# Optimization experiments

Measured on AMD Instinct MI355X. Metric: run time of the kernel, lower is better.

Reference implementation:

```python
import jax, jax.numpy as jnp
import numpy as np


def setup_inputs() -> dict:
    key = jax.random.key(0)
    ks = jax.random.split(key, 10)
    B, S, D = 16, 2048, 256
    return {
        "x": jax.random.normal(ks[0], (B, S, D), dtype=jnp.float32),
        "noise": jax.random.normal(ks[1], (B, S, D), dtype=jnp.float32),
        "alpha1": jax.random.normal(ks[2], (D,), dtype=jnp.float32),
        "alpha2": jax.random.normal(ks[3], (D,), dtype=jnp.float32),
        "W_ttt": jax.random.normal(ks[4], (D, D), dtype=jnp.float32),
        "W_proj": jax.random.normal(ks[5], (D, D), dtype=jnp.float32),
        "ff_alpha": jax.random.normal(ks[6], (D,), dtype=jnp.float32),
        "ff_beta": jax.random.normal(ks[7], (D,), dtype=jnp.float32),
        "ff_gamma": jax.random.normal(ks[8], (1,), dtype=jnp.float32),
        "ff_eta": jax.random.normal(ks[9], (1,), dtype=jnp.float32),
    }


def _ttt(W, m, noise):
    # m, noise: [B, S, D]; sequential SGD on W over the sequence axis.
    B, S, D = m.shape
    scale = 2.0 / (B * D)  # d(mse)/d(pred) factor

    def step(W, inp):
        state, eps = inp                      # [B, D] each
        train = state + eps
        diff = train @ W.T - state            # pred - label, [B, D]
        grad = scale * (diff.T @ train)       # dL/dW, [D, D]
        Wn = W - 0.01 * grad
        return Wn, state @ Wn.T               # readout with updated W

    _, outs = jax.lax.scan(step, W, (jnp.swapaxes(m, 0, 1), jnp.swapaxes(noise, 0, 1)))
    return jnp.swapaxes(outs, 0, 1)           # [B, S, D]


def reference(x, noise, alpha1, alpha2, W_ttt, W_proj, ff_alpha, ff_beta, ff_gamma, ff_eta):
    # memory path: VecDyT norm then TTT (readouts are detached in torch)
    m = jnp.tanh(alpha1 * x)
    mem = jax.lax.stop_gradient(_ttt(W_ttt, m, noise))

    # feedforward path: VecDyT norm then FFUnit
    v = jnp.tanh(alpha2 * x)
    u = ff_gamma * jax.nn.gelu(ff_alpha * v, approximate=False) + ff_eta * jnp.sin(ff_beta * v)
    g = u * (v @ W_proj.T)

    return mem + g
```

## Files before the change

kernel.cpp:

```cpp
#include <hip/hip_runtime.h>

typedef unsigned short u16;
typedef unsigned int u32;
typedef __attribute__((ext_vector_type(8))) short bf16x8;
typedef __attribute__((ext_vector_type(4))) float f32x4;

#define SB 16
#define SS 2048
#define SD 256
#define CC 16
#define NCH (SS / CC)
#define KAPPA 4.8828125e-6f
#define RP 24
#define SLOT 65536

__device__ __forceinline__ u16 f2bf(float f) {
  u32 u = __float_as_uint(f);
  u = (u + 0x7FFFu + ((u >> 16) & 1u)) >> 16;
  return (u16)u;
}
__device__ __forceinline__ float bf2f(u16 u) { return __uint_as_float((u32)u << 16); }

__device__ __forceinline__ bf16x8 ldfrag(const u16* p) {
  union { uint4 u; bf16x8 f; } cv;
  cv.u = *(const uint4*)p;
  return cv.f;
}
__device__ __forceinline__ bf16x8 asfrag(uint4 q) {
  union { uint4 u; bf16x8 f; } cv;
  cv.u = q;
  return cv.f;
}
__device__ __forceinline__ f32x4 mfma16(bf16x8 a, bf16x8 b, f32x4 c) {
  return __builtin_amdgcn_mfma_f32_16x16x32_bf16(a, b, c, 0, 0, 0);
}

__global__ __launch_bounds__(256) void prep_kernel(
    const float* __restrict__ x, const float* __restrict__ noise,
    const float* __restrict__ a1,
    u16* __restrict__ train, u16* __restrict__ state, u16* __restrict__ trainT) {
  size_t i4 = (size_t)blockIdx.x * 256 + threadIdx.x;
  size_t base = i4 * 4;
  int d = (int)(base & 255);
  int t = (int)((base >> 8) & 2047);
  int b = (int)(base >> 19);
  float4 xv = *(const float4*)(x + base);
  float4 nv = *(const float4*)(noise + base);
  float4 av = *(const float4*)(a1 + d);
  float m0 = tanhf(av.x * xv.x);
  float m1 = tanhf(av.y * xv.y);
  float m2 = tanhf(av.z * xv.z);
  float m3 = tanhf(av.w * xv.w);
  size_t dst = ((size_t)t * SB + b) * SD + d;
  ushort4 tr, st;
  tr.x = f2bf(m0 + nv.x); tr.y = f2bf(m1 + nv.y);
  tr.z = f2bf(m2 + nv.z); tr.w = f2bf(m3 + nv.w);
  st.x = f2bf(m0); st.y = f2bf(m1); st.z = f2bf(m2); st.w = f2bf(m3);
  *(ushort4*)(train + dst) = tr;
  *(ushort4*)(state + dst) = st;
  size_t tb = ((size_t)t * SD + d) * SB + b;
  trainT[tb + 0 * SB] = tr.x;
  trainT[tb + 1 * SB] = tr.y;
  trainT[tb + 2 * SB] = tr.z;
  trainT[tb + 3 * SB] = tr.w;
}

__global__ __launch_bounds__(256) void gram2ff_kernel(
    const u16* __restrict__ tr, const u16* __restrict__ st,
    u16* __restrict__ AG, u16* __restrict__ LbG,
    const float* __restrict__ x, const float* __restrict__ a2,
    const float* __restrict__ Wp, const float* __restrict__ ffa,
    const float* __restrict__ ffb, const float* __restrict__ ffg_,
    const float* __restrict__ ffe_, float* __restrict__ out) {
  __shared__ float As[32][68];
  __shared__ float Bs[32][68];
  const int tid = threadIdx.x;

  if (blockIdx.x < 2048) {
    const int cb = blockIdx.x;
    const int c = cb >> 4, t = cb & 15;
    const int lane = tid & 63, wv = tid >> 6;
    const int lr = lane & 15, lq = lane >> 4;
    const size_t Tt = (size_t)cb;
    bf16x8 trF[8], stF[8];
#pragma unroll
    for (int k = 0; k < 8; ++k) {
      trF[k] = ldfrag(tr + (Tt * 16 + lr) * 256 + k * 32 + lq * 8);
      stF[k] = ldfrag(st + (Tt * 16 + lr) * 256 + k * 32 + lq * 8);
    }
    for (int ii = 0; ii < 2; ++ii) {
      const int sp = wv + ii * 4;
      u16* dA = AG + ((size_t)cb * 8 + sp) * 512;
      u16* dL = LbG + ((size_t)cb * 8 + sp) * 512;
#pragma unroll
      for (int h = 0; h < 2; ++h) {
        const int s = 2 * sp + h;
        f32x4 accA = {0.f, 0.f, 0.f, 0.f}, accL = {0.f, 0.f, 0.f, 0.f};
        if (s <= t) {
          const u16* bsrc = tr + ((size_t)(c * 16 + s) * 16 + lr) * 256 + lq * 8;
#pragma unroll
          for (int k = 0; k < 8; ++k) {
            bf16x8 bk = ldfrag(bsrc + k * 32);
            if (s < t) accA = mfma16(trF[k], bk, accA);
            accL = mfma16(stF[k], bk, accL);
          }
        }
#pragma unroll
        for (int r = 0; r < 4; ++r) {
          int idx = (lq * 4 + r) * 32 + h * 16 + lr;
          dA[idx] = (s < t) ? f2bf(accA[r]) : (u16)0;
          dL[idx] = (s <= t) ? f2bf(accL[r]) : (u16)0;
        }
      }
    }
    return;
  }

  const int fb = blockIdx.x - 2048;
  const int gm0 = (fb >> 2) * 64;
  const int gn0 = (fb & 3) * 64;
  const int tm = tid & 15, tn = tid >> 4;
  const int lr = tid & 63;
  const int lq = tid >> 6;
  float acc[4][4];
#pragma unroll
  for (int i = 0; i < 4; i++)
#pragma unroll
    for (int j = 0; j < 4; j++) acc[i][j] = 0.f;

  for (int k0 = 0; k0 < 256; k0 += 32) {
    {
      const float* xp = x + (size_t)(gm0 + lr) * 256 + k0 + lq * 8;
      float4 v0 = *(const float4*)(xp);
      float4 v1 = *(const float4*)(xp + 4);
      const float* ap = a2 + k0 + lq * 8;
      float4 a0 = *(const float4*)(ap);
      float4 a1v = *(const float4*)(ap + 4);
      As[lq * 8 + 0][lr] = tanhf(a0.x * v0.x);
      As[lq * 8 + 1][lr] = tanhf(a0.y * v0.y);
      As[lq * 8 + 2][lr] = tanhf(a0.z * v0.z);
      As[lq * 8 + 3][lr] = tanhf(a0.w * v0.w);
      As[lq * 8 + 4][lr] = tanhf(a1v.x * v1.x);
      As[lq * 8 + 5][lr] = tanhf(a1v.y * v1.y);
      As[lq * 8 + 6][lr] = tanhf(a1v.z * v1.z);
      As[lq * 8 + 7][lr] = tanhf(a1v.w * v1.w);
      const float* wp = Wp + (size_t)(gn0 + lr) * 256 + k0 + lq * 8;
      float4 w0 = *(const float4*)(wp);
      float4 w1 = *(const float4*)(wp + 4);
      Bs[lq * 8 + 0][lr] = w0.x; Bs[lq * 8 + 1][lr] = w0.y;
      Bs[lq * 8 + 2][lr] = w0.z; Bs[lq * 8 + 3][lr] = w0.w;
      Bs[lq * 8 + 4][lr] = w1.x; Bs[lq * 8 + 5][lr] = w1.y;
      Bs[lq * 8 + 6][lr] = w1.z; Bs[lq * 8 + 7][lr] = w1.w;
    }
    __syncthreads();
#pragma unroll
    for (int k = 0; k < 32; ++k) {
      float4 av4 = *(const float4*)&As[k][tm * 4];
      float4 bv4 = *(const float4*)&Bs[k][tn * 4];
      float a[4] = {av4.x, av4.y, av4.z, av4.w};
      float b[4] = {bv4.x, bv4.y, bv4.z, bv4.w};
#pragma unroll
      for (int i = 0; i < 4; i++)
#pragma unroll
        for (int j = 0; j < 4; j++) acc[i][j] += a[i] * b[j];
    }
    __syncthreads();
  }
  const float ga = ffg_[0], et = ffe_[0];
#pragma unroll
  for (int ii = 0; ii < 4; ++ii) {
    int row = gm0 + tm * 4 + ii;
    int col = gn0 + tn * 4;
    float4 xv = *(const float4*)(x + (size_t)row * 256 + col);
    float4 fa = *(const float4*)(ffa + col);
    float4 fb4 = *(const float4*)(ffb + col);
    float4 a2v = *(const float4*)(a2 + col);
    float xs[4] = {xv.x, xv.y, xv.z, xv.w};
    float fas[4] = {fa.x, fa.y, fa.z, fa.w};
    float fbs[4] = {fb4.x, fb4.y, fb4.z, fb4.w};
    float a2s[4] = {a2v.x, a2v.y, a2v.z, a2v.w};
    float res[4];
#pragma unroll
    for (int j = 0; j < 4; ++j) {
      float v = tanhf(a2s[j] * xs[j]);
      float z = fas[j] * v;
      float gelu = 0.5f * z * (1.0f + erff(z * 0.70710678118654752f));
      float u = ga * gelu + et * sinf(fbs[j] * v);
      res[j] = u * acc[ii][j];
    }
    float4 o; o.x = res[0]; o.y = res[1]; o.z = res[2]; o.w = res[3];
    *(float4*)(out + (size_t)row * 256 + col) = o;
  }
}

__global__ __launch_bounds__(512) void phaseA_kernel(
    const u16* __restrict__ tr, const u16* __restrict__ st,
    const u16* __restrict__ trT, const u16* __restrict__ AG,
    u16* __restrict__ Dt, u16* __restrict__ Db, u16* __restrict__ Qb) {
  __shared__ u16 StT[CC][16 * RP];
  __shared__ u16 YtL[CC][16 * RP];
  __shared__ u16 ZtL[CC][16 * RP];
  const int tid = threadIdx.x;
  const int lane = tid & 63;
  const int w = tid >> 6;
  const int d1b = blockIdx.x;
  const int c = blockIdx.y;
  const int lr = lane & 15;
  const int lq = lane >> 4;

  uint4 agR[2][8];
#pragma unroll
  for (int u = 0; u < 2; ++u) {
    const u16* ag = AG + ((size_t)(c * 16 + w + 8 * u) * 8) * 512 + lr * 32 + lq * 8;
#pragma unroll
    for (int sp = 0; sp < 8; ++sp) agR[u][sp] = *(const uint4*)(ag + sp * 512);
  }
  u16 sraw[2][4];
  float xs[2][4];
#pragma unroll
  for (int u = 0; u < 2; ++u) {
    const size_t T = (size_t)c * CC + w + 8 * u;
    ushort4 pk;
#pragma unroll
    for (int r = 0; r < 4; ++r) {
      size_t idx = (T * 16 + lq * 4 + r) * 256 + d1b * 16 + lr;
      sraw[u][r] = st[idx];
      xs[u][r] = bf2f(tr[idx]);
      ((u16*)&pk)[r] = sraw[u][r];
    }
    *(ushort4*)(&StT[w + 8 * u][lr * RP + lq * 4]) = pk;
  }
  __syncthreads();

#pragma unroll
  for (int u = 0; u < 2; ++u) {
    f32x4 a1 = {0.f, 0.f, 0.f, 0.f}, a2 = {0.f, 0.f, 0.f, 0.f};
#pragma unroll
    for (int sp = 0; sp < 8; ++sp) {
      const int s0 = 2 * sp + (lq >> 1);
      bf16x8 xb = ldfrag(trT + ((size_t)(c * CC + s0) * 256 + d1b * 16 + lr) * 16 +
                         (lq & 1) * 8);
      bf16x8 sb = ldfrag(&StT[s0][lr * RP + (lq & 1) * 8]);
      a1 = mfma16(asfrag(agR[u][sp]), xb, a1);
      a2 = mfma16(asfrag(agR[u][sp]), sb, a2);
    }
    ushort4 py, pz;
#pragma unroll
    for (int r = 0; r < 4; ++r) {
      ((u16*)&py)[r] = f2bf(xs[u][r] - KAPPA * a1[r]);
      ((u16*)&pz)[r] = f2bf(bf2f(sraw[u][r]) - KAPPA * a2[r]);
    }
    *(ushort4*)(&YtL[w + 8 * u][lr * RP + lq * 4]) = py;
    *(ushort4*)(&ZtL[w + 8 * u][lr * RP + lq * 4]) = pz;
  }
  __syncthreads();

  bf16x8 yf[8], zf[8];
#pragma unroll
  for (int sp = 0; sp < 8; ++sp) {
    yf[sp] = ldfrag(&YtL[2 * sp + (lq >> 1)][lr * RP + (lq & 1) * 8]);
    zf[sp] = ldfrag(&ZtL[2 * sp + (lq >> 1)][lr * RP + (lq & 1) * 8]);
  }
  const size_t base = (size_t)c * SLOT;
#pragma unroll
  for (int u = 0; u < 2; ++u) {
    const int d2b = w + 8 * u;
    f32x4 da = {0.f, 0.f, 0.f, 0.f}, qa = {0.f, 0.f, 0.f, 0.f};
#pragma unroll
    for (int sp = 0; sp < 8; ++sp) {
      bf16x8 xb = ldfrag(trT + ((size_t)(c * CC + 2 * sp + (lq >> 1)) * 256 +
                                d2b * 16 + lr) * 16 + (lq & 1) * 8);
      da = mfma16(yf[sp], xb, da);
      qa = mfma16(zf[sp], xb, qa);
    }
    ushort4 dpk;
#pragma unroll
    for (int r = 0; r < 4; ++r) {
      const u16 dv = f2bf(-KAPPA * da[r]);
      ((u16*)&dpk)[r] = dv;
      Db[base + (size_t)(d1b * 16 + lq * 4 + r) * 256 + d2b * 16 + lr] = dv;
      Qb[base + (size_t)(d1b * 16 + lq * 4 + r) * 256 + d2b * 16 + lr] =
          f2bf(KAPPA * qa[r]);
    }
    *(ushort4*)(Dt + base + (size_t)(d2b * 16 + lr) * 256 + d1b * 16 + lq * 4) = dpk;
  }
}

__global__ __launch_bounds__(512) void kq_kernel(
    const u16* __restrict__ Dt, u16* __restrict__ Qb, int lev) {
  const int qn = blockIdx.x >> 4, rb = blockIdx.x & 15;
  const int half = 1 << (lev - 1);
  const int blk = qn >> (lev - 1), win = qn & (half - 1);
  const int i = blk * half * 2 + half + win;
  const int j = blk * half * 2 + half - 1;
  u16* Qi = Qb + (size_t)i * SLOT;
  const u16* Qj = Qb + (size_t)j * SLOT;
  const u16* Dti = Dt + (size_t)i * SLOT;
  const int lane = threadIdx.x & 63, w = threadIdx.x >> 6;
  const int lr = lane & 15, lq = lane >> 4;
  bf16x8 aq[8];
#pragma unroll
  for (int kb = 0; kb < 8; ++kb)
    aq[kb] = ldfrag(Qj + (size_t)(rb * 16 + lr) * 256 + kb * 32 + lq * 8);
#pragma unroll
  for (int u = 0; u < 2; ++u) {
    const int cb = w + 8 * u;
    f32x4 acc = {0.f, 0.f, 0.f, 0.f};
#pragma unroll
    for (int kb = 0; kb < 8; ++kb) {
      bf16x8 bf = ldfrag(Dti + (size_t)(cb * 16 + lr) * 256 + kb * 32 + lq * 8);
      acc = mfma16(aq[kb], bf, acc);
    }
#pragma unroll
    for (int r = 0; r < 4; ++r) {
      size_t idx = (size_t)(rb * 16 + lq * 4 + r) * 256 + cb * 16 + lr;
      float v = acc[r] + bf2f(Qj[idx]) + bf2f(Qi[idx]);
      Qi[idx] = f2bf(v);
    }
  }
}

__global__ __launch_bounds__(512) void kdt_kernel(
    u16* __restrict__ Dt, u16* __restrict__ Db, int lev) {
  const int qn = blockIdx.x >> 4, rb = blockIdx.x & 15;
  const int half = 1 << (lev - 1);
  const int blk = qn >> (lev - 1), win = qn & (half - 1);
  const int i = blk * half * 2 + half + win;
  const int j = blk * half * 2 + half - 1;
  u16* Dti = Dt + (size_t)i * SLOT;
  const u16* Dtj = Dt + (size_t)j * SLOT;
  u16* Dbi = Db + (size_t)i * SLOT;
  const u16* Dbj = Db + (size_t)j * SLOT;
  const int lane = threadIdx.x & 63, w = threadIdx.x >> 6;
  const int lr = lane & 15, lq = lane >> 4;
  bf16x8 ad[8];
#pragma unroll
  for (int kb = 0; kb < 8; ++kb)
    ad[kb] = ldfrag(Dti + (size_t)(rb * 16 + lr) * 256 + kb * 32 + lq * 8);
  float oldv[2][4];
#pragma unroll
  for (int u = 0; u < 2; ++u) {
    const int cb = w + 8 * u;
#pragma unroll
    for (int r = 0; r < 4; ++r) {
      size_t idx = (size_t)(rb * 16 + lq * 4 + r) * 256 + cb * 16 + lr;
      oldv[u][r] = bf2f(Dtj[idx]) + bf2f(Dti[idx]);
    }
  }
  __syncthreads();
#pragma unroll
  for (int u = 0; u < 2; ++u) {
    const int cb = w + 8 * u;
    f32x4 acc = {0.f, 0.f, 0.f, 0.f};
#pragma unroll
    for (int kb = 0; kb < 8; ++kb) {
      bf16x8 bf = ldfrag(Dbj + (size_t)(cb * 16 + lr) * 256 + kb * 32 + lq * 8);
      acc = mfma16(ad[kb], bf, acc);
    }
    ushort4 mir;
#pragma unroll
    for (int r = 0; r < 4; ++r) {
      const u16 nv = f2bf(acc[r] + oldv[u][r]);
      ((u16*)&mir)[r] = nv;
      Dti[(size_t)(rb * 16 + lq * 4 + r) * 256 + cb * 16 + lr] = nv;
    }
    *(ushort4*)(Dbi + (size_t)(cb * 16 + lr) * 256 + rb * 16 + lq * 4) = mir;
  }
}

__global__ __launch_bounds__(512) void wstart_kernel(
    const float* __restrict__ Wttt, const u16* __restrict__ Dt,
    const u16* __restrict__ Qb, u16* __restrict__ Wsb) {
  const int c = blockIdx.x;
  const int tid = threadIdx.x;
  const int lane = tid & 63, w = tid >> 6;
  const int lr = lane & 15, lq = lane >> 4;
  if (c == 0) {
    for (int i = tid; i < SLOT / 4; i += 512) {
      float4 v = *(const float4*)(Wttt + (size_t)i * 4);
      ushort4 o;
      o.x = f2bf(v.x); o.y = f2bf(v.y); o.z = f2bf(v.z); o.w = f2bf(v.w);
      *(ushort4*)(Wsb + (size_t)i * 4) = o;
    }
    return;
  }
  const size_t ex = (size_t)(c - 1) * SLOT;
  u16* Wc = Wsb + (size_t)c * SLOT;
#pragma unroll
  for (int ui = 0; ui < 2; ++ui) {
    const int rb = w + 8 * ui;
    bf16x8 wf[8];
#pragma unroll
    for (int kb = 0; kb < 8; ++kb) {
      const float* wp = Wttt + (size_t)(rb * 16 + lr) * 256 + kb * 32 + lq * 8;
      float4 w0 = *(const float4*)(wp);
      float4 w1 = *(const float4*)(wp + 4);
      union { u16 s[8]; bf16x8 f; } cv;
      cv.s[0] = f2bf(w0.x); cv.s[1] = f2bf(w0.y);
      cv.s[2] = f2bf(w0.z); cv.s[3] = f2bf(w0.w);
      cv.s[4] = f2bf(w1.x); cv.s[5] = f2bf(w1.y);
      cv.s[6] = f2bf(w1.z); cv.s[7] = f2bf(w1.w);
      wf[kb] = cv.f;
    }
    for (int cb = 0; cb < 16; ++cb) {
      f32x4 acc = {0.f, 0.f, 0.f, 0.f};
#pragma unroll
      for (int kb = 0; kb < 8; ++kb) {
        bf16x8 bf = ldfrag(Dt + ex + (size_t)(cb * 16 + lr) * 256 + kb * 32 + lq * 8);
        acc = mfma16(wf[kb], bf, acc);
      }
#pragma unroll
      for (int r = 0; r < 4; ++r) {
        size_t idx = (size_t)(rb * 16 + lq * 4 + r) * 256 + cb * 16 + lr;
        float v = Wttt[idx] + acc[r] + bf2f(Qb[ex + idx]);
        Wc[idx] = f2bf(v);
      }
    }
  }
}

__global__ __launch_bounds__(512) void phaseC_kernel(
    const u16* __restrict__ tr, const u16* __restrict__ st,
    const u16* __restrict__ AG, const u16* __restrict__ LbG,
    const u16* __restrict__ Wsb, float* __restrict__ out) {
  __shared__ u16 RpL[CC][16 * RP];
  __shared__ u16 DpL[CC][16 * RP];
  __shared__ u16 WbL[16][268];

  const int tid = threadIdx.x;
  const int lane = tid & 63;
  const int w = tid >> 6;
  const int d1b = blockIdx.x;
  const int c = blockIdx.y;
  const int lr = lane & 15;
  const int lq = lane >> 4;

  {
    const int row = tid >> 5, col = (tid & 31) * 8;
    *(uint4*)&WbL[row][col] =
        *(const uint4*)(Wsb + (size_t)c * SLOT + (size_t)(d1b * 16 + row) * 256 + col);
  }
  __syncthreads();

  uint4 agR[2][8];
#pragma unroll
  for (int u = 0; u < 2; ++u) {
    const u16* ag = AG + ((size_t)(c * 16 + w + 8 * u) * 8) * 512 + lr * 32 + lq * 8;
#pragma unroll
    for (int sp = 0; sp < 8; ++sp) agR[u][sp] = *(const uint4*)(ag + sp * 512);
  }
  uint4 trR[2][8], stR[2][8];
  float sub[2][4];
#pragma unroll
  for (int u = 0; u < 2; ++u) {
    const size_t T = (size_t)c * CC + w + 8 * u;
    const u16* trt = tr + (T * 16 + lr) * 256 + lq * 8;
    const u16* stt = st + (T * 16 + lr) * 256 + lq * 8;
#pragma unroll
    for (int k = 0; k < 8; ++k) {
      trR[u][k] = *(const uint4*)(trt + k * 32);
      stR[u][k] = *(const uint4*)(stt + k * 32);
    }
#pragma unroll
    for (int r = 0; r < 4; ++r)
      sub[u][r] = bf2f(st[(T * 16 + lq * 4 + r) * 256 + d1b * 16 + lr]);
  }

  f32x4 rhsF[2], qF[2];
#pragma unroll
  for (int u = 0; u < 2; ++u) {
    f32x4 racc = {0.f, 0.f, 0.f, 0.f}, qacc = {0.f, 0.f, 0.f, 0.f};
#pragma unroll
    for (int k = 0; k < 8; ++k) {
      bf16x8 wb = ldfrag(&WbL[lr][k * 32 + lq * 8]);
      racc = mfma16(asfrag(trR[u][k]), wb, racc);
      qacc = mfma16(asfrag(stR[u][k]), wb, qacc);
    }
#pragma unroll
    for (int r = 0; r < 4; ++r) racc[r] -= sub[u][r];
    rhsF[u] = racc; qF[u] = qacc;
    ushort4 pk;
    pk.x = f2bf(racc.x); pk.y = f2bf(racc.y);
    pk.z = f2bf(racc.z); pk.w = f2bf(racc.w);
    *(ushort4*)(&RpL[w + 8 * u][lr * RP + lq * 4]) = pk;
  }
  __syncthreads();

  uint4 lbR[2][8];
#pragma unroll
  for (int u = 0; u < 2; ++u) {
    const u16* lb = LbG + ((size_t)(c * 16 + w + 8 * u) * 8) * 512 + lr * 32 + lq * 8;
#pragma unroll
    for (int sp = 0; sp < 8; ++sp) lbR[u][sp] = *(const uint4*)(lb + sp * 512);
  }

#pragma unroll
  for (int u = 0; u < 2; ++u) {
    f32x4 acc = {0.f, 0.f, 0.f, 0.f};
#pragma unroll
    for (int sp = 0; sp < 8; ++sp) {
      bf16x8 bf = ldfrag(&RpL[2 * sp + (lq >> 1)][lr * RP + (lq & 1) * 8]);
      acc = mfma16(asfrag(agR[u][sp]), bf, acc);
    }
    ushort4 pk;
#pragma unroll
    for (int r = 0; r < 4; ++r) {
      float dv = rhsF[u][r] - KAPPA * acc[r];
      ((u16*)&pk)[r] = f2bf(-KAPPA * dv);
    }
    *(ushort4*)(&DpL[w + 8 * u][lr * RP + lq * 4]) = pk;
  }
  __syncthreads();

  float gp[2][4];
#pragma unroll
  for (int u = 0; u < 2; ++u) {
    const size_t T = (size_t)c * CC + w + 8 * u;
#pragma unroll
    for (int r = 0; r < 4; ++r)
      gp[u][r] = out[((size_t)(lq * 4 + r) * SS + T) * SD + d1b * 16 + lr];
  }
#pragma unroll
  for (int u = 0; u < 2; ++u) {
    const size_t T = (size_t)c * CC + w + 8 * u;
    f32x4 acc = qF[u];
#pragma unroll
    for (int sp = 0; sp < 8; ++sp) {
      bf16x8 bf = ldfrag(&DpL[2 * sp + (lq >> 1)][lr * RP + (lq & 1) * 8]);
      acc = mfma16(asfrag(lbR[u][sp]), bf, acc);
    }
#pragma unroll
    for (int r = 0; r < 4; ++r) {
      size_t oi = ((size_t)(lq * 4 + r) * SS + T) * SD + d1b * 16 + lr;
      out[oi] = acc[r] + gp[u][r];
    }
  }
}

extern "C" void kernel_launch(void* const* d_in, const int* in_sizes, int n_in,
                              void* d_out, int out_size, void* d_ws, size_t ws_size,
                              hipStream_t stream) {
  const float* x     = (const float*)d_in[0];
  const float* noise = (const float*)d_in[1];
  const float* a1    = (const float*)d_in[2];
  const float* a2    = (const float*)d_in[3];
  const float* Wttt  = (const float*)d_in[4];
  const float* Wproj = (const float*)d_in[5];
  const float* ffa   = (const float*)d_in[6];
  const float* ffb   = (const float*)d_in[7];
  const float* ffg   = (const float*)d_in[8];
  const float* ffe   = (const float*)d_in[9];
  float* out = (float*)d_out;

  const size_t N = (size_t)SB * SS * SD;
  u16* tr  = (u16*)d_ws;
  u16* st  = tr + N;
  u16* trT = st + N;
  u16* AG  = trT + N;
  u16* LbG = AG + N;
  u16* Dt  = LbG + N;
  u16* Qb  = Dt + N;
  u16* Db  = Qb + N;
  u16* Wsb = trT;

  prep_kernel<<<8192, 256, 0, stream>>>(x, noise, a1, tr, st, trT);
  gram2ff_kernel<<<4096, 256, 0, stream>>>(tr, st, AG, LbG,
                                           x, a2, Wproj, ffa, ffb, ffg, ffe, out);
  phaseA_kernel<<<dim3(16, 128), 512, 0, stream>>>(tr, st, trT, AG, Dt, Db, Qb);
  for (int lev = 1; lev <= 7; ++lev) {
    kq_kernel<<<1024, 512, 0, stream>>>(Dt, Qb, lev);
    kdt_kernel<<<1024, 512, 0, stream>>>(Dt, Db, lev);
  }
  wstart_kernel<<<128, 512, 0, stream>>>(Wttt, Dt, Qb, Wsb);
  phaseC_kernel<<<dim3(16, 128), 512, 0, stream>>>(tr, st, AG, LbG, Wsb, out);
}
```

Measured before the change: 919.5 us.

## Move feedforward GEMM to split-bf16 MFMA and swizzle block indices

```diff
diff --git a/kernel.cpp b/kernel.cpp
--- a/kernel.cpp
+++ b/kernel.cpp
@@ -37,8 +37,9 @@
 
 __global__ __launch_bounds__(256) void prep_kernel(
     const float* __restrict__ x, const float* __restrict__ noise,
-    const float* __restrict__ a1,
-    u16* __restrict__ train, u16* __restrict__ state, u16* __restrict__ trainT) {
+    const float* __restrict__ a1, const float* __restrict__ a2,
+    u16* __restrict__ train, u16* __restrict__ state, u16* __restrict__ trainT,
+    u16* __restrict__ vh, u16* __restrict__ vl) {
   size_t i4 = (size_t)blockIdx.x * 256 + threadIdx.x;
   size_t base = i4 * 4;
   int d = (int)(base & 255);
@@ -47,6 +48,7 @@
   float4 xv = *(const float4*)(x + base);
   float4 nv = *(const float4*)(noise + base);
   float4 av = *(const float4*)(a1 + d);
+  float4 a2v = *(const float4*)(a2 + d);
   float m0 = tanhf(av.x * xv.x);
   float m1 = tanhf(av.y * xv.y);
   float m2 = tanhf(av.z * xv.z);
@@ -63,17 +65,40 @@
   trainT[tb + 1 * SB] = tr.y;
   trainT[tb + 2 * SB] = tr.z;
   trainT[tb + 3 * SB] = tr.w;
+  float v0 = tanhf(a2v.x * xv.x);
+  float v1 = tanhf(a2v.y * xv.y);
+  float v2 = tanhf(a2v.z * xv.z);
+  float v3 = tanhf(a2v.w * xv.w);
+  ushort4 h, l;
+  h.x = f2bf(v0); l.x = f2bf(v0 - bf2f(h.x));
+  h.y = f2bf(v1); l.y = f2bf(v1 - bf2f(h.y));
+  h.z = f2bf(v2); l.z = f2bf(v2 - bf2f(h.z));
+  h.w = f2bf(v3); l.w = f2bf(v3 - bf2f(h.w));
+  *(ushort4*)(vh + base) = h;
+  *(ushort4*)(vl + base) = l;
+}
+
+__global__ __launch_bounds__(256) void wsplit_kernel(
+    const float* __restrict__ Wp, u16* __restrict__ Wph, u16* __restrict__ Wpl) {
+  size_t i = ((size_t)blockIdx.x * 256 + threadIdx.x) * 4;
+  float4 v = *(const float4*)(Wp + i);
+  ushort4 h, l;
+  h.x = f2bf(v.x); l.x = f2bf(v.x - bf2f(h.x));
+  h.y = f2bf(v.y); l.y = f2bf(v.y - bf2f(h.y));
+  h.z = f2bf(v.z); l.z = f2bf(v.z - bf2f(h.z));
+  h.w = f2bf(v.w); l.w = f2bf(v.w - bf2f(h.w));
+  *(ushort4*)(Wph + i) = h;
+  *(ushort4*)(Wpl + i) = l;
 }
 
 __global__ __launch_bounds__(256) void gram2ff_kernel(
     const u16* __restrict__ tr, const u16* __restrict__ st,
     u16* __restrict__ AG, u16* __restrict__ LbG,
-    const float* __restrict__ x, const float* __restrict__ a2,
-    const float* __restrict__ Wp, const float* __restrict__ ffa,
-    const float* __restrict__ ffb, const float* __restrict__ ffg_,
-    const float* __restrict__ ffe_, float* __restrict__ out) {
-  __shared__ float As[32][68];
-  __shared__ float Bs[32][68];
+    const u16* __restrict__ vh, const u16* __restrict__ vl,
+    const u16* __restrict__ Wph, const u16* __restrict__ Wpl,
+    const float* __restrict__ ffa, const float* __restrict__ ffb,
+    const float* __restrict__ ffg_, const float* __restrict__ ffe_,
+    float* __restrict__ out) {
   const int tid = threadIdx.x;
 
   if (blockIdx.x < 2048) {
@@ -117,79 +142,46 @@
   }
 
   const int fb = blockIdx.x - 2048;
-  const int gm0 = (fb >> 2) * 64;
-  const int gn0 = (fb & 3) * 64;
-  const int tm = tid & 15, tn = tid >> 4;
-  const int lr = tid & 63;
-  const int lq = tid >> 6;
-  float acc[4][4];
-#pragma unroll
-  for (int i = 0; i < 4; i++)
-#pragma unroll
-    for (int j = 0; j < 4; j++) acc[i][j] = 0.f;
-
-  for (int k0 = 0; k0 < 256; k0 += 32) {
-    {
-      const float* xp = x + (size_t)(gm0 + lr) * 256 + k0 + lq * 8;
-      float4 v0 = *(const float4*)(xp);
-      float4 v1 = *(const float4*)(xp + 4);
-      const float* ap = a2 + k0 + lq * 8;
-      float4 a0 = *(const float4*)(ap);
-      float4 a1v = *(const float4*)(ap + 4);
-      As[lq * 8 + 0][lr] = tanhf(a0.x * v0.x);
-      As[lq * 8 + 1][lr] = tanhf(a0.y * v0.y);
-      As[lq * 8 + 2][lr] = tanhf(a0.z * v0.z);
-      As[lq * 8 + 3][lr] = tanhf(a0.w * v0.w);
-      As[lq * 8 + 4][lr] = tanhf(a1v.x * v1.x);
-      As[lq * 8 + 5][lr] = tanhf(a1v.y * v1.y);
-      As[lq * 8 + 6][lr] = tanhf(a1v.z * v1.z);
-      As[lq * 8 + 7][lr] = tanhf(a1v.w * v1.w);
-      const float* wp = Wp + (size_t)(gn0 + lr) * 256 + k0 + lq * 8;
-      float4 w0 = *(const float4*)(wp);
-      float4 w1 = *(const float4*)(wp + 4);
-      Bs[lq * 8 + 0][lr] = w0.x; Bs[lq * 8 + 1][lr] = w0.y;
-      Bs[lq * 8 + 2][lr] = w0.z; Bs[lq * 8 + 3][lr] = w0.w;
-      Bs[lq * 8 + 4][lr] = w1.x; Bs[lq * 8 + 5][lr] = w1.y;
-      Bs[lq * 8 + 6][lr] = w1.z; Bs[lq * 8 + 7][lr] = w1.w;
-    }
-    __syncthreads();
-#pragma unroll
-    for (int k = 0; k < 32; ++k) {
-      float4 av4 = *(const float4*)&As[k][tm * 4];
-      float4 bv4 = *(const float4*)&Bs[k][tn * 4];
-      float a[4] = {av4.x, av4.y, av4.z, av4.w};
-      float b[4] = {bv4.x, bv4.y, bv4.z, bv4.w};
-#pragma unroll
-      for (int i = 0; i < 4; i++)
-#pragma unroll
-        for (int j = 0; j < 4; j++) acc[i][j] += a[i] * b[j];
-    }
-    __syncthreads();
+  const int gm0 = ((fb & 7) + 8 * (fb >> 5)) * 64;
+  const int gn0 = ((fb >> 3) & 3) * 64;
+  const int lane = tid & 63, w = tid >> 6;
+  const int lr = lane & 15, lq = lane >> 4;
+
+  bf16x8 ah[8], al[8];
+  {
+    const u16* vhp = vh + (size_t)(gm0 + w * 16 + lr) * 256 + lq * 8;
+    const u16* vlp = vl + (size_t)(gm0 + w * 16 + lr) * 256 + lq * 8;
+#pragma unroll
+    for (int kb = 0; kb < 8; ++kb) {
+      ah[kb] = ldfrag(vhp + kb * 32);
+      al[kb] = ldfrag(vlp + kb * 32);
+    }
   }
   const float ga = ffg_[0], et = ffe_[0];
 #pragma unroll
-  for (int ii = 0; ii < 4; ++ii) {
-    int row = gm0 + tm * 4 + ii;
-    int col = gn0 + tn * 4;
-    float4 xv = *(const float4*)(x + (size_t)row * 256 + col);
-    float4 fa = *(const float4*)(ffa + col);
-    float4 fb4 = *(const float4*)(ffb + col);
-    float4 a2v = *(const float4*)(a2 + col);
-    float xs[4] = {xv.x, xv.y, xv.z, xv.w};
-    float fas[4] = {fa.x, fa.y, fa.z, fa.w};
-    float fbs[4] = {fb4.x, fb4.y, fb4.z, fb4.w};
-    float a2s[4] = {a2v.x, a2v.y, a2v.z, a2v.w};
-    float res[4];
-#pragma unroll
-    for (int j = 0; j < 4; ++j) {
-      float v = tanhf(a2s[j] * xs[j]);
-      float z = fas[j] * v;
+  for (int cb = 0; cb < 4; ++cb) {
+    const u16* bhp = Wph + (size_t)(gn0 + cb * 16 + lr) * 256 + lq * 8;
+    const u16* blp = Wpl + (size_t)(gn0 + cb * 16 + lr) * 256 + lq * 8;
+    f32x4 acc = {0.f, 0.f, 0.f, 0.f};
+#pragma unroll
+    for (int kb = 0; kb < 8; ++kb) {
+      bf16x8 bh = ldfrag(bhp + kb * 32);
+      bf16x8 bl = ldfrag(blp + kb * 32);
+      acc = mfma16(ah[kb], bh, acc);
+      acc = mfma16(al[kb], bh, acc);
+      acc = mfma16(ah[kb], bl, acc);
+    }
+#pragma unroll
+    for (int r = 0; r < 4; ++r) {
+      const int row = gm0 + w * 16 + lq * 4 + r;
+      const int col = gn0 + cb * 16 + lr;
+      const size_t vi = (size_t)row * 256 + col;
+      float v = bf2f(vh[vi]) + bf2f(vl[vi]);
+      float z = ffa[col] * v;
       float gelu = 0.5f * z * (1.0f + erff(z * 0.70710678118654752f));
-      float u = ga * gelu + et * sinf(fbs[j] * v);
-      res[j] = u * acc[ii][j];
-    }
-    float4 o; o.x = res[0]; o.y = res[1]; o.z = res[2]; o.w = res[3];
-    *(float4*)(out + (size_t)row * 256 + col) = o;
+      float u = ga * gelu + et * sinf(ffb[col] * v);
+      out[vi] = u * acc[r];
+    }
   }
 }
 
@@ -203,8 +195,9 @@
   const int tid = threadIdx.x;
   const int lane = tid & 63;
   const int w = tid >> 6;
-  const int d1b = blockIdx.x;
-  const int c = blockIdx.y;
+  const int id = blockIdx.x;
+  const int c = (id & 7) + 8 * (id >> 7);
+  const int d1b = (id >> 3) & 15;
   const int lr = lane & 15;
   const int lq = lane >> 4;
 
@@ -288,7 +281,9 @@
 
 __global__ __launch_bounds__(512) void kq_kernel(
     const u16* __restrict__ Dt, u16* __restrict__ Qb, int lev) {
-  const int qn = blockIdx.x >> 4, rb = blockIdx.x & 15;
+  const int id = blockIdx.x;
+  const int qn = (id & 7) + 8 * (id >> 7);
+  const int rb = (id >> 3) & 15;
   const int half = 1 << (lev - 1);
   const int blk = qn >> (lev - 1), win = qn & (half - 1);
   const int i = blk * half * 2 + half + win;
@@ -322,7 +317,9 @@
 
 __global__ __launch_bounds__(512) void kdt_kernel(
     u16* __restrict__ Dt, u16* __restrict__ Db, int lev) {
-  const int qn = blockIdx.x >> 4, rb = blockIdx.x & 15;
+  const int id = blockIdx.x;
+  const int qn = (id & 7) + 8 * (id >> 7);
+  const int rb = (id >> 3) & 15;
   const int half = 1 << (lev - 1);
   const int blk = qn >> (lev - 1), win = qn & (half - 1);
   const int i = blk * half * 2 + half + win;
@@ -430,8 +427,9 @@
   const int tid = threadIdx.x;
   const int lane = tid & 63;
   const int w = tid >> 6;
-  const int d1b = blockIdx.x;
-  const int c = blockIdx.y;
+  const int id = blockIdx.x;
+  const int c = (id & 7) + 8 * (id >> 7);
+  const int d1b = (id >> 3) & 15;
   const int lr = lane & 15;
   const int lq = lane >> 4;
 
@@ -562,15 +560,20 @@
   u16* Qb  = Dt + N;
   u16* Db  = Qb + N;
   u16* Wsb = trT;
-
-  prep_kernel<<<8192, 256, 0, stream>>>(x, noise, a1, tr, st, trT);
-  gram2ff_kernel<<<4096, 256, 0, stream>>>(tr, st, AG, LbG,
-                                           x, a2, Wproj, ffa, ffb, ffg, ffe, out);
-  phaseA_kernel<<<dim3(16, 128), 512, 0, stream>>>(tr, st, trT, AG, Dt, Db, Qb);
+  u16* vhB = Dt;
+  u16* vlB = Qb;
+  u16* Wph = Db;
+  u16* Wpl = Db + SLOT;
+
+  prep_kernel<<<8192, 256, 0, stream>>>(x, noise, a1, a2, tr, st, trT, vhB, vlB);
+  wsplit_kernel<<<64, 256, 0, stream>>>(Wproj, Wph, Wpl);
+  gram2ff_kernel<<<4096, 256, 0, stream>>>(tr, st, AG, LbG, vhB, vlB, Wph, Wpl,
+                                           ffa, ffb, ffg, ffe, out);
+  phaseA_kernel<<<2048, 512, 0, stream>>>(tr, st, trT, AG, Dt, Db, Qb);
   for (int lev = 1; lev <= 7; ++lev) {
     kq_kernel<<<1024, 512, 0, stream>>>(Dt, Qb, lev);
     kdt_kernel<<<1024, 512, 0, stream>>>(Dt, Db, lev);
   }
   wstart_kernel<<<128, 512, 0, stream>>>(Wttt, Dt, Qb, Wsb);
-  phaseC_kernel<<<dim3(16, 128), 512, 0, stream>>>(tr, st, AG, LbG, Wsb, out);
-}
+  phaseC_kernel<<<2048, 512, 0, stream>>>(tr, st, AG, LbG, Wsb, out);
+}
```

New measurement: 894.4 us. 2.7% less time.
